# Kernel tuning notes

Hardware: AMD Instinct MI355X
Metric: run time of the kernel (lower is better)

The kernel has to match this reference:

```python
import jax, jax.numpy as jnp
import numpy as np

NUM_GRAPHS = 2048
NODES_PER_GRAPH = 256
N_NODES = NUM_GRAPHS * NODES_PER_GRAPH
N_EDGES = 2 * N_NODES
F_IN = 768
HID = 128
N_CLS = 2


def setup_inputs() -> dict:
    key = jax.random.key(0)
    ks = jax.random.split(key, 12)
    x = jax.random.normal(ks[0], (N_NODES, F_IN), dtype=jnp.float32)
    edge_index = jax.random.randint(ks[1], (2, N_EDGES), 0, N_NODES, dtype=jnp.int32)
    batch = jnp.repeat(jnp.arange(NUM_GRAPHS, dtype=jnp.int32), NODES_PER_GRAPH)
    s = 1.0 / np.sqrt(F_IN)
    sh = 1.0 / np.sqrt(HID)
    s2h = 1.0 / np.sqrt(2 * HID)
    return {
        "x": x,
        "edge_index": edge_index,
        "batch": batch,
        # SAGEConv: lin_l (aggregated neighbors, with bias) + lin_r (root, no bias)
        "W_l": jax.random.uniform(ks[2], (F_IN, HID), jnp.float32, -s, s),
        "b_l": jax.random.uniform(ks[3], (HID,), jnp.float32, -s, s),
        "W_r": jax.random.uniform(ks[4], (F_IN, HID), jnp.float32, -s, s),
        "W0": jax.random.uniform(ks[5], (F_IN, HID), jnp.float32, -s, s),
        "b0": jax.random.uniform(ks[6], (HID,), jnp.float32, -s, s),
        "W1": jax.random.uniform(ks[7], (2 * HID, HID), jnp.float32, -s2h, s2h),
        "b1": jax.random.uniform(ks[8], (HID,), jnp.float32, -s2h, s2h),
        "W2": jax.random.uniform(ks[9], (HID, N_CLS), jnp.float32, -sh, sh),
        "b2": jax.random.uniform(ks[10], (HID,), jnp.float32, -sh, sh)[:N_CLS],
    }


def reference(x, edge_index, batch, W_l, b_l, W_r, W0, b0, W1, b1, W2, b2):
    n = x.shape[0]
    src, dst = edge_index[0], edge_index[1]
    # SAGEConv with mean aggregation: gather -> segment mean -> transform
    msg_sum = jax.ops.segment_sum(x[src], dst, num_segments=n)      # [N, F]
    cnt = jax.ops.segment_sum(jnp.ones((src.shape[0],), x.dtype), dst, num_segments=n)
    agg = msg_sum / jnp.maximum(cnt, 1.0)[:, None]
    h = jax.nn.relu(agg @ W_l + b_l + x @ W_r)                       # [N, H]
    # global max pool per graph
    pooled = jax.ops.segment_max(h, batch, num_segments=NUM_GRAPHS)  # [G, H]
    # root (news) node = first node of each graph (batch is sorted)
    roots = jnp.searchsorted(batch, jnp.arange(NUM_GRAPHS, dtype=batch.dtype))
    news = jax.nn.relu(x[roots] @ W0 + b0)                           # [G, H]
    z = jax.nn.relu(jnp.concatenate([pooled, news], axis=1) @ W1 + b1)
    return jax.nn.log_softmax(z @ W2 + b2, axis=-1)                  # [G, 2]
```

## Files before the change

### kernel.cpp

```cpp
#include <hip/hip_runtime.h>

#define NGRAPH 2048
#define NPG 256
#define NNODE (NGRAPH*NPG)
#define NEDGE (2*NNODE)
#define FIN 768
#define HID 128
#define SLOTS 64
#define BK 32
#define NKT (FIN/BK)

typedef __bf16 bf16x8 __attribute__((ext_vector_type(8)));
typedef float f32x4 __attribute__((ext_vector_type(4)));

__device__ __forceinline__ float bflo(unsigned v) {
    return __uint_as_float((v & 0xffffu) << 16);
}
__device__ __forceinline__ float bfhi(unsigned v) {
    return __uint_as_float(v & 0xffff0000u);
}

__global__ __launch_bounds__(256) void k_prep(
    const float* __restrict__ Wl, const float* __restrict__ Wr,
    __bf16* __restrict__ WbT, int* __restrict__ deg)
{
    int idx = blockIdx.x * 256 + threadIdx.x;
    deg[idx] = 0;
    if (idx < 256 * FIN) {
        int n = idx / FIN;
        int k = idx - n * FIN;
        float v = (n < HID) ? Wl[k * HID + n] : Wr[k * HID + (n - HID)];
        WbT[idx] = (__bf16)v;
    }
}

__global__ __launch_bounds__(512, 1) void k_gemm(
    const float* __restrict__ X, const __bf16* __restrict__ WbT,
    __bf16* __restrict__ Yl, __bf16* __restrict__ Yr,
    const int* __restrict__ ei, int* __restrict__ deg, int* __restrict__ elist)
{
    __shared__ __align__(16) char sm[65536];
    const int t = threadIdx.x;

    {
        int e = blockIdx.x * 512 + t;
        int src = ei[e];
        int dst = ei[NEDGE + e];
        int pos = atomicAdd(deg + dst, 1);
        if (pos < SLOTS) elist[(size_t)pos * NNODE + dst] = src;
    }

    const int lane = t & 63;
    const int w = t >> 6;
    const int wr = w >> 2;
    const int wc = w & 3;
    const size_t node0 = (size_t)blockIdx.x * 256;

    f32x4 acc[8][4];
#pragma unroll
    for (int m = 0; m < 8; ++m)
#pragma unroll
        for (int n = 0; n < 4; ++n)
            acc[m][n] = (f32x4){0.f, 0.f, 0.f, 0.f};

    const int arow = t >> 1;
    const int ak = (t & 1) * 16;
    const float* asrc = X + (node0 + arow) * FIN + ak;
    const int axr = ((arow >> 1) & 3) << 4;
    const int aoff0 = arow * 64 + ((ak * 2) ^ axr);
    const int aoff1 = arow * 64 + ((ak * 2 + 16) ^ axr);

#define STAGE_B(k0, dst)                                                    \
    {                                                                       \
        _Pragma("unroll")                                                   \
        for (int r = 0; r < 2; ++r) {                                       \
            int idx = r * 512 + t;                                          \
            int bn = idx >> 2;                                              \
            int bj = idx & 3;                                               \
            int koff = (bj ^ ((bn >> 1) & 3)) << 3;                         \
            const __bf16* g = WbT + bn * FIN + (k0) + koff;                 \
            __builtin_amdgcn_global_load_lds(                               \
                (__attribute__((address_space(1))) void*)g,                 \
                (__attribute__((address_space(3))) void*)((dst) + idx * 16),\
                16, 0, 0);                                                  \
        }                                                                   \
    }

    {
        const f32x4* s4 = (const f32x4*)asrc;
        f32x4 p0 = s4[0], p1 = s4[1], p2 = s4[2], p3 = s4[3];
        STAGE_B(0, sm + 32768);
        bf16x8 h0, h1;
#pragma unroll
        for (int i = 0; i < 4; ++i) {
            h0[i]     = (__bf16)p0[i];
            h0[4 + i] = (__bf16)p1[i];
            h1[i]     = (__bf16)p2[i];
            h1[4 + i] = (__bf16)p3[i];
        }
        *(bf16x8*)(sm + aoff0) = h0;
        *(bf16x8*)(sm + aoff1) = h1;
    }
    __syncthreads();

    int cur = 0;
    for (int kt = 0; kt < NKT; ++kt) {
        char* sAc = sm + cur * 16384;
        char* sBc = sm + 32768 + cur * 16384;
        char* sAn = sm + (cur ^ 1) * 16384;
        char* sBn = sm + 32768 + (cur ^ 1) * 16384;
        const bool more = (kt + 1 < NKT);

        f32x4 q0, q1, q2, q3;
        if (more) {
            const f32x4* s4 = (const f32x4*)(asrc + (kt + 1) * BK);
            q0 = s4[0]; q1 = s4[1]; q2 = s4[2]; q3 = s4[3];
            STAGE_B((kt + 1) * BK, sBn);
        }

        const int kb = (lane >> 4) << 4;
        bf16x8 a[8], b[4];
#pragma unroll
        for (int m = 0; m < 8; ++m) {
            int row = wr * 128 + m * 16 + (lane & 15);
            a[m] = *(const bf16x8*)(sAc + row * 64 + (kb ^ (((row >> 1) & 3) << 4)));
        }
#pragma unroll
        for (int n = 0; n < 4; ++n) {
            int row = wc * 64 + n * 16 + (lane & 15);
            b[n] = *(const bf16x8*)(sBc + row * 64 + (kb ^ (((row >> 1) & 3) << 4)));
        }
#pragma unroll
        for (int m = 0; m < 8; ++m)
#pragma unroll
            for (int n = 0; n < 4; ++n)
                acc[m][n] = __builtin_amdgcn_mfma_f32_16x16x32_bf16(
                    a[m], b[n], acc[m][n], 0, 0, 0);

        if (more) {
            bf16x8 h0, h1;
#pragma unroll
            for (int i = 0; i < 4; ++i) {
                h0[i]     = (__bf16)q0[i];
                h0[4 + i] = (__bf16)q1[i];
                h1[i]     = (__bf16)q2[i];
                h1[4 + i] = (__bf16)q3[i];
            }
            *(bf16x8*)(sAn + aoff0) = h0;
            *(bf16x8*)(sAn + aoff1) = h1;
        }
        __syncthreads();
        cur ^= 1;
    }

#pragma unroll
    for (int m = 0; m < 8; ++m) {
        const int rbase = wr * 128 + m * 16 + ((lane >> 4) << 2);
#pragma unroll
        for (int n = 0; n < 4; ++n) {
            const int col = wc * 64 + n * 16 + (lane & 15);
            __bf16* dst = (col < HID) ? Yl : Yr;
            const int c = col & (HID - 1);
#pragma unroll
            for (int j = 0; j < 4; ++j)
                dst[(node0 + rbase + j) * HID + c] = (__bf16)acc[m][n][j];
        }
    }
#undef STAGE_B
}

__global__ __launch_bounds__(512) void k_fused(
    const int* __restrict__ deg, const int* __restrict__ elist,
    const __bf16* __restrict__ Yl, const __bf16* __restrict__ Yr,
    const float* __restrict__ bl, const float* __restrict__ X,
    const float* __restrict__ W0, const float* __restrict__ b0,
    const float* __restrict__ W1, const float* __restrict__ b1,
    const float* __restrict__ W2, const float* __restrict__ b2,
    float* __restrict__ out)
{
    __shared__ int   sdeg[NPG];
    __shared__ int   sel[4 * NPG];
    __shared__ float xs[FIN];
    __shared__ float red[8 * HID];
    __shared__ float nred[4 * HID];
    __shared__ float cat[2 * HID];
    __shared__ float zs[HID];

    const int g = blockIdx.x;
    const int t = threadIdx.x;
    const size_t gbase = (size_t)g * NPG;

    if (t < NPG) sdeg[t] = deg[gbase + t];
#pragma unroll
    for (int r = 0; r < 2; ++r) {
        int idx = r * 512 + t;
        sel[idx] = elist[(size_t)(idx >> 8) * NNODE + gbase + (idx & 255)];
    }
    for (int i = t; i < FIN; i += 512) xs[i] = X[gbase * FIN + i];
    __syncthreads();

    const int l = t & 63;
    const int sub = t >> 6;
    const int d2 = l * 2;
    const float bl0 = bl[d2], bl1 = bl[d2 + 1];
    const unsigned short* yl = (const unsigned short*)Yl;
    const unsigned short* yr = (const unsigned short*)Yr;
    float m0 = -3.0e38f, m1 = -3.0e38f;

    for (int i0 = sub; i0 < NPG; i0 += 16) {
        const int iA = i0, iB = i0 + 8;
        const int dgA = sdeg[iA], dgB = sdeg[iB];
        unsigned vA[4], vB[4];
        float mkA[4], mkB[4];
#pragma unroll
        for (int j = 0; j < 4; ++j) {
            int sA = sel[j * NPG + iA];
            int sB = sel[j * NPG + iB];
            mkA[j] = (j < dgA) ? 1.f : 0.f;
            mkB[j] = (j < dgB) ? 1.f : 0.f;
            sA = (j < dgA) ? sA : 0;
            sB = (j < dgB) ? sB : 0;
            vA[j] = *(const unsigned*)(yl + (size_t)sA * HID + d2);
            vB[j] = *(const unsigned*)(yl + (size_t)sB * HID + d2);
        }
        const unsigned vyA = *(const unsigned*)(yr + (gbase + iA) * HID + d2);
        const unsigned vyB = *(const unsigned*)(yr + (gbase + iB) * HID + d2);
        float s0A = 0.f, s1A = 0.f, s0B = 0.f, s1B = 0.f;
#pragma unroll
        for (int j = 0; j < 4; ++j) {
            s0A = fmaf(mkA[j], bflo(vA[j]), s0A);
            s1A = fmaf(mkA[j], bfhi(vA[j]), s1A);
            s0B = fmaf(mkB[j], bflo(vB[j]), s0B);
            s1B = fmaf(mkB[j], bfhi(vB[j]), s1B);
        }
        if (dgA > 4) {
            const int dgc = dgA < SLOTS ? dgA : SLOTS;
            for (int j = 4; j < dgc; ++j) {
                int s = elist[(size_t)j * NNODE + gbase + iA];
                unsigned v = *(const unsigned*)(yl + (size_t)s * HID + d2);
                s0A += bflo(v); s1A += bfhi(v);
            }
        }
        if (dgB > 4) {
            const int dgc = dgB < SLOTS ? dgB : SLOTS;
            for (int j = 4; j < dgc; ++j) {
                int s = elist[(size_t)j * NNODE + gbase + iB];
                unsigned v = *(const unsigned*)(yl + (size_t)s * HID + d2);
                s0B += bflo(v); s1B += bfhi(v);
            }
        }
        const float invA = 1.f / fmaxf((float)dgA, 1.f);
        const float invB = 1.f / fmaxf((float)dgB, 1.f);
        float h0 = fmaf(s0A, invA, bl0) + bflo(vyA);
        float h1 = fmaf(s1A, invA, bl1) + bfhi(vyA);
        m0 = fmaxf(m0, fmaxf(h0, 0.f));
        m1 = fmaxf(m1, fmaxf(h1, 0.f));
        h0 = fmaf(s0B, invB, bl0) + bflo(vyB);
        h1 = fmaf(s1B, invB, bl1) + bfhi(vyB);
        m0 = fmaxf(m0, fmaxf(h0, 0.f));
        m1 = fmaxf(m1, fmaxf(h1, 0.f));
    }
    red[sub * HID + d2] = m0;
    red[sub * HID + d2 + 1] = m1;

    {
        const int q = t >> 7;
        const int d = t & 127;
        const int kb = q * 192;
        float a0 = 0.f, a1 = 0.f, a2 = 0.f, a3 = 0.f;
        for (int k = kb; k < kb + 192; k += 4) {
            a0 = fmaf(xs[k + 0], W0[(k + 0) * HID + d], a0);
            a1 = fmaf(xs[k + 1], W0[(k + 1) * HID + d], a1);
            a2 = fmaf(xs[k + 2], W0[(k + 2) * HID + d], a2);
            a3 = fmaf(xs[k + 3], W0[(k + 3) * HID + d], a3);
        }
        nred[q * HID + d] = (a0 + a1) + (a2 + a3);
    }
    __syncthreads();

    if (t < HID) {
        float v = red[t];
#pragma unroll
        for (int s = 1; s < 8; ++s) v = fmaxf(v, red[s * HID + t]);
        cat[t] = v;
        float nw = (nred[t] + nred[HID + t]) + (nred[2 * HID + t] + nred[3 * HID + t]);
        cat[HID + t] = fmaxf(nw + b0[t], 0.f);
    }
    __syncthreads();

    if (t < HID) {
        float a0 = 0.f, a1 = 0.f, a2 = 0.f, a3 = 0.f;
        for (int k = 0; k < 2 * HID; k += 4) {
            a0 = fmaf(cat[k + 0], W1[(k + 0) * HID + t], a0);
            a1 = fmaf(cat[k + 1], W1[(k + 1) * HID + t], a1);
            a2 = fmaf(cat[k + 2], W1[(k + 2) * HID + t], a2);
            a3 = fmaf(cat[k + 3], W1[(k + 3) * HID + t], a3);
        }
        zs[t] = fmaxf((a0 + a1) + (a2 + a3) + b1[t], 0.f);
    }
    __syncthreads();

    if (t < 64) {
        float z0 = zs[t * 2], z1 = zs[t * 2 + 1];
        float p0 = fmaf(z0, W2[t * 4 + 0], z1 * W2[t * 4 + 2]);
        float p1 = fmaf(z0, W2[t * 4 + 1], z1 * W2[t * 4 + 3]);
#pragma unroll
        for (int off = 32; off; off >>= 1) {
            p0 += __shfl_down(p0, off);
            p1 += __shfl_down(p1, off);
        }
        if (t == 0) {
            float l0 = p0 + b2[0], l1 = p1 + b2[1];
            float mx = fmaxf(l0, l1);
            float lse = mx + logf(expf(l0 - mx) + expf(l1 - mx));
            out[(size_t)g * 2 + 0] = l0 - lse;
            out[(size_t)g * 2 + 1] = l1 - lse;
        }
    }
}

extern "C" void kernel_launch(void* const* d_in, const int* in_sizes, int n_in,
                              void* d_out, int out_size, void* d_ws, size_t ws_size,
                              hipStream_t stream)
{
    const float* x   = (const float*)d_in[0];
    const int*   ei  = (const int*)d_in[1];
    const float* W_l = (const float*)d_in[3];
    const float* b_l = (const float*)d_in[4];
    const float* W_r = (const float*)d_in[5];
    const float* W0  = (const float*)d_in[6];
    const float* b0  = (const float*)d_in[7];
    const float* W1  = (const float*)d_in[8];
    const float* b1  = (const float*)d_in[9];
    const float* W2  = (const float*)d_in[10];
    const float* b2  = (const float*)d_in[11];
    float* out = (float*)d_out;

    char* ws = (char*)d_ws;
    size_t off = 0;
    auto alloc = [&](size_t bytes) {
        char* p = ws + off;
        off += (bytes + 511) & ~(size_t)511;
        return p;
    };
    __bf16* WbT   = (__bf16*)alloc((size_t)256 * FIN * 2);
    __bf16* Yl    = (__bf16*)alloc((size_t)NNODE * HID * 2);
    __bf16* Yr    = (__bf16*)alloc((size_t)NNODE * HID * 2);
    int*    deg   = (int*)alloc((size_t)NNODE * 4);
    int*    elist = (int*)alloc((size_t)NNODE * SLOTS * 4);
    if (off > ws_size) return;

    k_prep<<<NNODE / 256, 256, 0, stream>>>(W_l, W_r, WbT, deg);
    k_gemm<<<NNODE / 256, 512, 0, stream>>>(x, WbT, Yl, Yr, ei, deg, elist);
    k_fused<<<NGRAPH, 512, 0, stream>>>(deg, elist, Yl, Yr, b_l, x, W0, b0,
                                        W1, b1, W2, b2, out);
}
```

Before: 635.8 us.

## Move root-node W0 projection to a separate bf16 MFMA kernel and widen gather loads

The per-graph scalar fp32 x[root]@W0 dot product is taken out of the fused pooling kernel and placed in a new batched MFMA kernel, k_news, that processes 64 graphs per block. k_news uses a bf16 copy of W0 built in k_prep. The neighbour gather now loads 4 bf16 features per lane, with two half-waves covering different nodes. The overflow-degree loop becomes a wave-uniform masked loop instead of per-node branches. This adds a kernel launch and rounds the news-path inputs to bf16, in exchange for cutting repeated fp32 W0 reads from every graph block.

After: 649.2 us. 2.1% more time.

```diff
diff --git a/kernel.cpp b/kernel.cpp
--- a/kernel.cpp
+++ b/kernel.cpp
@@ -11,6 +11,7 @@
 #define NKT (FIN/BK)
 
 typedef __bf16 bf16x8 __attribute__((ext_vector_type(8)));
+typedef __bf16 bf16x4 __attribute__((ext_vector_type(4)));
 typedef float f32x4 __attribute__((ext_vector_type(4)));
 
 __device__ __forceinline__ float bflo(unsigned v) {
@@ -22,14 +23,18 @@
 
 __global__ __launch_bounds__(256) void k_prep(
     const float* __restrict__ Wl, const float* __restrict__ Wr,
-    __bf16* __restrict__ WbT, int* __restrict__ deg)
+    const float* __restrict__ W0, __bf16* __restrict__ WbT,
+    int* __restrict__ deg)
 {
     int idx = blockIdx.x * 256 + threadIdx.x;
     deg[idx] = 0;
-    if (idx < 256 * FIN) {
+    if (idx < 384 * FIN) {
         int n = idx / FIN;
         int k = idx - n * FIN;
-        float v = (n < HID) ? Wl[k * HID + n] : Wr[k * HID + (n - HID)];
+        float v;
+        if (n < HID)            v = Wl[k * HID + n];
+        else if (n < 2 * HID)   v = Wr[k * HID + (n - HID)];
+        else                    v = W0[k * HID + (n - 2 * HID)];
         WbT[idx] = (__bf16)v;
     }
 }
@@ -169,20 +174,98 @@
 #undef STAGE_B
 }
 
+__global__ __launch_bounds__(512) void k_news(
+    const float* __restrict__ X, const __bf16* __restrict__ W0bT,
+    const float* __restrict__ b0, float* __restrict__ news)
+{
+    __shared__ __align__(16) char sm[12288];
+    const int t = threadIdx.x;
+    const int lane = t & 63;
+    const int w = t >> 6;
+    const int wr = w >> 2;
+    const int wc = w & 3;
+    const int g0 = blockIdx.x * 64;
+
+    f32x4 acc[2][2];
+#pragma unroll
+    for (int m = 0; m < 2; ++m)
+#pragma unroll
+        for (int n = 0; n < 2; ++n)
+            acc[m][n] = (f32x4){0.f, 0.f, 0.f, 0.f};
+
+    const int arow = t >> 3;
+    const int ak = (t & 7) * 4;
+    const float* asrc = X + (size_t)(g0 + arow) * (NPG * FIN) + ak;
+    const int aoff = arow * 64 + (((ak * 2) ^ (((arow >> 1) & 3) << 4)));
+
+    for (int kt = 0; kt < NKT; ++kt) {
+        const int k0 = kt * BK;
+        __syncthreads();
+        {
+            f32x4 p = *(const f32x4*)(asrc + k0);
+            bf16x4 h;
+#pragma unroll
+            for (int i = 0; i < 4; ++i) h[i] = (__bf16)p[i];
+            *(bf16x4*)(sm + aoff) = h;
+        }
+        {
+            int bn = t >> 2;
+            int bj = t & 3;
+            int koff = (bj ^ ((bn >> 1) & 3)) << 3;
+            const __bf16* g = W0bT + bn * FIN + k0 + koff;
+            __builtin_amdgcn_global_load_lds(
+                (__attribute__((address_space(1))) void*)g,
+                (__attribute__((address_space(3))) void*)(sm + 4096 + t * 16),
+                16, 0, 0);
+        }
+        __syncthreads();
+
+        const int kb = (lane >> 4) << 4;
+        bf16x8 a[2], b[2];
+#pragma unroll
+        for (int m = 0; m < 2; ++m) {
+            int row = wr * 32 + m * 16 + (lane & 15);
+            a[m] = *(const bf16x8*)(sm + row * 64 + (kb ^ (((row >> 1) & 3) << 4)));
+        }
+#pragma unroll
+        for (int n = 0; n < 2; ++n) {
+            int row = wc * 32 + n * 16 + (lane & 15);
+            b[n] = *(const bf16x8*)(sm + 4096 + row * 64 + (kb ^ (((row >> 1) & 3) << 4)));
+        }
+#pragma unroll
+        for (int m = 0; m < 2; ++m)
+#pragma unroll
+            for (int n = 0; n < 2; ++n)
+                acc[m][n] = __builtin_amdgcn_mfma_f32_16x16x32_bf16(
+                    a[m], b[n], acc[m][n], 0, 0, 0);
+    }
+
+#pragma unroll
+    for (int m = 0; m < 2; ++m) {
+        const int rbase = wr * 32 + m * 16 + ((lane >> 4) << 2);
+#pragma unroll
+        for (int n = 0; n < 2; ++n) {
+            const int col = wc * 32 + n * 16 + (lane & 15);
+            const float bb = b0[col];
+#pragma unroll
+            for (int j = 0; j < 4; ++j)
+                news[(size_t)(g0 + rbase + j) * HID + col] =
+                    fmaxf(acc[m][n][j] + bb, 0.f);
+        }
+    }
+}
+
 __global__ __launch_bounds__(512) void k_fused(
     const int* __restrict__ deg, const int* __restrict__ elist,
     const __bf16* __restrict__ Yl, const __bf16* __restrict__ Yr,
-    const float* __restrict__ bl, const float* __restrict__ X,
-    const float* __restrict__ W0, const float* __restrict__ b0,
+    const float* __restrict__ bl, const float* __restrict__ news,
     const float* __restrict__ W1, const float* __restrict__ b1,
     const float* __restrict__ W2, const float* __restrict__ b2,
     float* __restrict__ out)
 {
     __shared__ int   sdeg[NPG];
     __shared__ int   sel[4 * NPG];
-    __shared__ float xs[FIN];
     __shared__ float red[8 * HID];
-    __shared__ float nred[4 * HID];
     __shared__ float cat[2 * HID];
     __shared__ float zs[HID];
 
@@ -196,85 +279,102 @@
         int idx = r * 512 + t;
         sel[idx] = elist[(size_t)(idx >> 8) * NNODE + gbase + (idx & 255)];
     }
-    for (int i = t; i < FIN; i += 512) xs[i] = X[gbase * FIN + i];
     __syncthreads();
 
     const int l = t & 63;
     const int sub = t >> 6;
-    const int d2 = l * 2;
-    const float bl0 = bl[d2], bl1 = bl[d2 + 1];
-    const unsigned short* yl = (const unsigned short*)Yl;
-    const unsigned short* yr = (const unsigned short*)Yr;
-    float m0 = -3.0e38f, m1 = -3.0e38f;
-
-    for (int i0 = sub; i0 < NPG; i0 += 16) {
-        const int iA = i0, iB = i0 + 8;
-        const int dgA = sdeg[iA], dgB = sdeg[iB];
-        unsigned vA[4], vB[4];
-        float mkA[4], mkB[4];
+    const int half = l >> 5;
+    const int lj = l & 31;
+    const int d4 = lj * 4;
+    const float4 blv = *(const float4*)(bl + d4);
+    const uint2* yl2 = (const uint2*)Yl;
+    const uint2* yr2 = (const uint2*)Yr;
+
+    float m0 = -3.0e38f, m1 = -3.0e38f, m2 = -3.0e38f, m3 = -3.0e38f;
+
+    for (int k4 = 0; k4 < 8; ++k4) {
+        const int nA = sub + 8 * (4 * k4 + half);
+        const int nB = sub + 8 * (4 * k4 + 2 + half);
+        const int dgA = sdeg[nA], dgB = sdeg[nB];
+        int sA[4], sB[4];
 #pragma unroll
         for (int j = 0; j < 4; ++j) {
-            int sA = sel[j * NPG + iA];
-            int sB = sel[j * NPG + iB];
-            mkA[j] = (j < dgA) ? 1.f : 0.f;
-            mkB[j] = (j < dgB) ? 1.f : 0.f;
-            sA = (j < dgA) ? sA : 0;
-            sB = (j < dgB) ? sB : 0;
-            vA[j] = *(const unsigned*)(yl + (size_t)sA * HID + d2);
-            vB[j] = *(const unsigned*)(yl + (size_t)sB * HID + d2);
-        }
-        const unsigned vyA = *(const unsigned*)(yr + (gbase + iA) * HID + d2);
-        const unsigned vyB = *(const unsigned*)(yr + (gbase + iB) * HID + d2);
-        float s0A = 0.f, s1A = 0.f, s0B = 0.f, s1B = 0.f;
+            int cA = sel[j * NPG + nA];
+            int cB = sel[j * NPG + nB];
+            sA[j] = (j < dgA) ? cA : 0;
+            sB[j] = (j < dgB) ? cB : 0;
+        }
+        uint2 vA[4], vB[4];
 #pragma unroll
         for (int j = 0; j < 4; ++j) {
-            s0A = fmaf(mkA[j], bflo(vA[j]), s0A);
-            s1A = fmaf(mkA[j], bfhi(vA[j]), s1A);
-            s0B = fmaf(mkB[j], bflo(vB[j]), s0B);
-            s1B = fmaf(mkB[j], bfhi(vB[j]), s1B);
-        }
-        if (dgA > 4) {
-            const int dgc = dgA < SLOTS ? dgA : SLOTS;
-            for (int j = 4; j < dgc; ++j) {
-                int s = elist[(size_t)j * NNODE + gbase + iA];
-                unsigned v = *(const unsigned*)(yl + (size_t)s * HID + d2);
-                s0A += bflo(v); s1A += bfhi(v);
-            }
-        }
-        if (dgB > 4) {
-            const int dgc = dgB < SLOTS ? dgB : SLOTS;
-            for (int j = 4; j < dgc; ++j) {
-                int s = elist[(size_t)j * NNODE + gbase + iB];
-                unsigned v = *(const unsigned*)(yl + (size_t)s * HID + d2);
-                s0B += bflo(v); s1B += bfhi(v);
-            }
+            vA[j] = yl2[(size_t)sA[j] * 32 + lj];
+            vB[j] = yl2[(size_t)sB[j] * 32 + lj];
+        }
+        const uint2 yA = yr2[(gbase + nA) * 32 + lj];
+        const uint2 yB = yr2[(gbase + nB) * 32 + lj];
+
+        float s0A = 0.f, s1A = 0.f, s2A = 0.f, s3A = 0.f;
+        float s0B = 0.f, s1B = 0.f, s2B = 0.f, s3B = 0.f;
+#pragma unroll
+        for (int j = 0; j < 4; ++j) {
+            const float mA = (j < dgA) ? 1.f : 0.f;
+            const float mB = (j < dgB) ? 1.f : 0.f;
+            s0A = fmaf(mA, bflo(vA[j].x), s0A);
+            s1A = fmaf(mA, bfhi(vA[j].x), s1A);
+            s2A = fmaf(mA, bflo(vA[j].y), s2A);
+            s3A = fmaf(mA, bfhi(vA[j].y), s3A);
+            s0B = fmaf(mB, bflo(vB[j].x), s0B);
+            s1B = fmaf(mB, bfhi(vB[j].x), s1B);
+            s2B = fmaf(mB, bflo(vB[j].y), s2B);
+            s3B = fmaf(mB, bfhi(vB[j].y), s3B);
+        }
+        int mx = dgA > dgB ? dgA : dgB;
+        mx = max(mx, __shfl_xor(mx, 32));
+        mx = mx < SLOTS ? mx : SLOTS;
+        for (int j = 4; j < mx; ++j) {
+            int cA = elist[(size_t)j * NNODE + gbase + nA];
+            int cB = elist[(size_t)j * NNODE + gbase + nB];
+            int eA = (j < dgA) ? cA : 0;
+            int eB = (j < dgB) ? cB : 0;
+            uint2 wA = yl2[(size_t)eA * 32 + lj];
+            uint2 wB = yl2[(size_t)eB * 32 + lj];
+            const float mA = (j < dgA) ? 1.f : 0.f;
+            const float mB = (j < dgB) ? 1.f : 0.f;
+            s0A = fmaf(mA, bflo(wA.x), s0A);
+            s1A = fmaf(mA, bfhi(wA.x), s1A);
+            s2A = fmaf(mA, bflo(wA.y), s2A);
+            s3A = fmaf(mA, bfhi(wA.y), s3A);
+            s0B = fmaf(mB, bflo(wB.x), s0B);
+            s1B = fmaf(mB, bfhi(wB.x), s1B);
+            s2B = fmaf(mB, bflo(wB.y), s2B);
+            s3B = fmaf(mB, bfhi(wB.y), s3B);
         }
         const float invA = 1.f / fmaxf((float)dgA, 1.f);
         const float invB = 1.f / fmaxf((float)dgB, 1.f);
-        float h0 = fmaf(s0A, invA, bl0) + bflo(vyA);
-        float h1 = fmaf(s1A, invA, bl1) + bfhi(vyA);
+        float h0 = fmaf(s0A, invA, blv.x) + bflo(yA.x);
+        float h1 = fmaf(s1A, invA, blv.y) + bfhi(yA.x);
+        float h2 = fmaf(s2A, invA, blv.z) + bflo(yA.y);
+        float h3 = fmaf(s3A, invA, blv.w) + bfhi(yA.y);
         m0 = fmaxf(m0, fmaxf(h0, 0.f));
         m1 = fmaxf(m1, fmaxf(h1, 0.f));
-        h0 = fmaf(s0B, invB, bl0) + bflo(vyB);
-        h1 = fmaf(s1B, invB, bl1) + bfhi(vyB);
+        m2 = fmaxf(m2, fmaxf(h2, 0.f));
+        m3 = fmaxf(m3, fmaxf(h3, 0.f));
+        h0 = fmaf(s0B, invB, blv.x) + bflo(yB.x);
+        h1 = fmaf(s1B, invB, blv.y) + bfhi(yB.x);
+        h2 = fmaf(s2B, invB, blv.z) + bflo(yB.y);
+        h3 = fmaf(s3B, invB, blv.w) + bfhi(yB.y);
         m0 = fmaxf(m0, fmaxf(h0, 0.f));
         m1 = fmaxf(m1, fmaxf(h1, 0.f));
-    }
-    red[sub * HID + d2] = m0;
-    red[sub * HID + d2 + 1] = m1;
-
-    {
-        const int q = t >> 7;
-        const int d = t & 127;
-        const int kb = q * 192;
-        float a0 = 0.f, a1 = 0.f, a2 = 0.f, a3 = 0.f;
-        for (int k = kb; k < kb + 192; k += 4) {
-            a0 = fmaf(xs[k + 0], W0[(k + 0) * HID + d], a0);
-            a1 = fmaf(xs[k + 1], W0[(k + 1) * HID + d], a1);
-            a2 = fmaf(xs[k + 2], W0[(k + 2) * HID + d], a2);
-            a3 = fmaf(xs[k + 3], W0[(k + 3) * HID + d], a3);
-        }
-        nred[q * HID + d] = (a0 + a1) + (a2 + a3);
+        m2 = fmaxf(m2, fmaxf(h2, 0.f));
+        m3 = fmaxf(m3, fmaxf(h3, 0.f));
+    }
+    m0 = fmaxf(m0, __shfl_xor(m0, 32));
+    m1 = fmaxf(m1, __shfl_xor(m1, 32));
+    m2 = fmaxf(m2, __shfl_xor(m2, 32));
+    m3 = fmaxf(m3, __shfl_xor(m3, 32));
+    if (half == 0) {
+        float4 mv = {m0, m1, m2, m3};
+        *(float4*)(red + sub * HID + d4) = mv;
     }
     __syncthreads();
 
@@ -283,8 +383,7 @@
 #pragma unroll
         for (int s = 1; s < 8; ++s) v = fmaxf(v, red[s * HID + t]);
         cat[t] = v;
-        float nw = (nred[t] + nred[HID + t]) + (nred[2 * HID + t] + nred[3 * HID + t]);
-        cat[HID + t] = fmaxf(nw + b0[t], 0.f);
+        cat[HID + t] = news[(size_t)g * HID + t];
     }
     __syncthreads();
 
@@ -343,15 +442,17 @@
         off += (bytes + 511) & ~(size_t)511;
         return p;
     };
-    __bf16* WbT   = (__bf16*)alloc((size_t)256 * FIN * 2);
+    __bf16* WbT   = (__bf16*)alloc((size_t)384 * FIN * 2);
     __bf16* Yl    = (__bf16*)alloc((size_t)NNODE * HID * 2);
     __bf16* Yr    = (__bf16*)alloc((size_t)NNODE * HID * 2);
     int*    deg   = (int*)alloc((size_t)NNODE * 4);
     int*    elist = (int*)alloc((size_t)NNODE * SLOTS * 4);
+    float*  news  = (float*)alloc((size_t)NGRAPH * HID * 4);
     if (off > ws_size) return;
 
-    k_prep<<<NNODE / 256, 256, 0, stream>>>(W_l, W_r, WbT, deg);
+    k_prep<<<NNODE / 256, 256, 0, stream>>>(W_l, W_r, W0, WbT, deg);
     k_gemm<<<NNODE / 256, 512, 0, stream>>>(x, WbT, Yl, Yr, ei, deg, elist);
-    k_fused<<<NGRAPH, 512, 0, stream>>>(deg, elist, Yl, Yr, b_l, x, W0, b0,
+    k_news<<<NGRAPH / 64, 512, 0, stream>>>(x, WbT + (size_t)256 * FIN, b0, news);
+    k_fused<<<NGRAPH, 512, 0, stream>>>(deg, elist, Yl, Yr, b_l, news,
                                         W1, b1, W2, b2, out);
 }
```
